# Optimization experiments

Measured on AMD Instinct MI355X. Metric: run time of the kernel, lower is better.

Reference implementation:

```python
import jax, jax.numpy as jnp
import numpy as np

N_E = 4096
E_DIM = 64
BETA = 0.25


def setup_inputs() -> dict:
    key = jax.random.key(0)
    k1, k2 = jax.random.split(key)
    z = jax.random.normal(k1, (16, E_DIM, 32, 32), dtype=jnp.float32)
    embedding = jax.random.normal(k2, (N_E, E_DIM), dtype=jnp.float32)
    return {"z": z, "embedding": embedding}


def reference(z, embedding):
    # b c h w -> b h w c
    zc = jnp.transpose(z, (0, 2, 3, 1))  # [B,H,W,C]
    B, H, W, C = zc.shape
    zf = zc.reshape(-1, C)  # [N, C]

    # Squared Euclidean distances (argmin is identical to cdist p=2 argmin)
    # d2[n,e] = |z|^2 - 2 z.e + |e|^2
    d2 = (
        jnp.sum(zf * zf, axis=1, keepdims=True)
        - 2.0 * (zf @ embedding.T)
        + jnp.sum(embedding * embedding, axis=1)[None, :]
    )  # [N, n_e]
    idx = jnp.argmin(d2, axis=1)  # [N]

    z_q = embedding[idx].reshape(B, H, W, C)

    # dist_p == 2 losses
    loss_d1 = jnp.mean((jax.lax.stop_gradient(z_q) - zc) ** 2)
    loss_d2 = jnp.mean((z_q - jax.lax.stop_gradient(zc)) ** 2)
    loss = BETA * loss_d1 + loss_d2

    # Straight-through estimator
    z_q = zc + jax.lax.stop_gradient(z_q - zc)

    indices = idx.reshape(B, H, W)
    z_q = jnp.transpose(z_q, (0, 3, 1, 2))  # b h w c -> b c h w
    return z_q, loss, indices
```

## Files before the change

### kernel.cpp

```cpp
#include <hip/hip_runtime.h>

typedef float f32x4 __attribute__((ext_vector_type(4)));
typedef float f32x16 __attribute__((ext_vector_type(16)));
typedef short bf16x8 __attribute__((ext_vector_type(8)));

#define HW_ 1024
#define NE_ 4096
#define CHW_ 65536
#define ZQ_SIZE 1048576
#define LOSS_OFF ZQ_SIZE
#define IDX_OFF (ZQ_SIZE + 1)
#define LOSS_SCALE (1.25f / 1048576.f)
#define EPS_GAP 0.1f

union FragU { unsigned u[4]; bf16x8 v; };

__device__ __forceinline__ unsigned umin_(unsigned a, unsigned b) { return a < b ? a : b; }
__device__ __forceinline__ unsigned umax_(unsigned a, unsigned b) { return a > b ? a : b; }

__device__ __forceinline__ void top2_(unsigned key, unsigned& s1, unsigned& s2) {
    unsigned t;
    asm("v_med3_u32 %0, %1, %2, %3" : "=v"(t) : "v"(key), "v"(s1), "v"(s2));
    s2 = t;
    s1 = umin_(s1, key);
}

__device__ __forceinline__ void split8(const float* v, FragU& hi, FragU& lo) {
#pragma unroll
    for (int p = 0; p < 4; p++) {
        float a = v[2 * p], b = v[2 * p + 1];
        unsigned ua = __float_as_uint(a), ub = __float_as_uint(b);
        hi.u[p] = (ua >> 16) | (ub & 0xFFFF0000u);
        float la = a - __uint_as_float(ua & 0xFFFF0000u);
        float lb = b - __uint_as_float(ub & 0xFFFF0000u);
        lo.u[p] = (__float_as_uint(la) >> 16) | (__float_as_uint(lb) & 0xFFFF0000u);
    }
}

__device__ __forceinline__ void gload_lds16(const void* g, void* l) {
    __builtin_amdgcn_global_load_lds(
        (const __attribute__((address_space(1))) unsigned*)g,
        (__attribute__((address_space(3))) unsigned*)l, 16, 0, 0);
}

__global__ __launch_bounds__(256) void vq_eprep(
        const float* __restrict__ emb, char* __restrict__ efrag,
        float* __restrict__ h_e, float* __restrict__ out) {
    const int bid = blockIdx.x, tid = threadIdx.x;
    if (bid < 128) {
        int u = bid * 256 + tid;
        int l = u & 63, ks = (u >> 6) & 3, t = u >> 8;
        int erow = t * 32 + (l & 31);
        int k0 = ks * 16 + (l >> 5) * 8;
        const float* ep = emb + (size_t)erow * 64 + k0;
        float4 ea = *(const float4*)(ep);
        float4 eb = *(const float4*)(ep + 4);
        float v[8];
        v[0] = -ea.x; v[1] = -ea.y; v[2] = -ea.z; v[3] = -ea.w;
        v[4] = -eb.x; v[5] = -eb.y; v[6] = -eb.z; v[7] = -eb.w;
        FragU hi, lo;
        split8(v, hi, lo);
        char* base = efrag + (size_t)t * 8192 + ks * 1024 + l * 16;
        *(FragU*)(base)        = hi;
        *(FragU*)(base + 4096) = lo;
    } else {
        int t = (bid - 128) * 256 + tid;
        const float4* er = (const float4*)(emb + (size_t)t * 64);
        float s = 0.f;
#pragma unroll
        for (int k = 0; k < 16; k++) {
            float4 e4 = er[k];
            s = fmaf(e4.x, e4.x, s); s = fmaf(e4.y, e4.y, s);
            s = fmaf(e4.z, e4.z, s); s = fmaf(e4.w, e4.w, s);
        }
        h_e[t] = 0.5f * s;
        if (t == 0) out[LOSS_OFF] = 0.f;
    }
}

__global__ __launch_bounds__(512) void vq_mfma(
        const float* __restrict__ z, const char* __restrict__ efrag,
        const float* __restrict__ h_e,
        unsigned* __restrict__ k1q, unsigned* __restrict__ k2q) {
    __shared__ char buf[2][32768];
    __shared__ __attribute__((aligned(16))) float sh_he[512];

    const int tid = threadIdx.x;
    const int lane = tid & 63;
    const int w = tid >> 6;
    const int col = lane & 31;
    const int kgrp = lane >> 5;
    const int es = blockIdx.x >> 5;
    const int rb = blockIdx.x & 31;
    const int e0t = es * 16;
    const int b = rb >> 1;
    const int row0 = rb * 512 + w * 64;

    sh_he[tid] = h_e[es * 512 + tid];

    {
        const char* src = efrag + (size_t)(e0t + (w >> 1)) * 8192
                          + (w & 1) * 4096 + lane * 16;
        char* dst = buf[0] + (w >> 1) * 8192 + (w & 1) * 4096;
#pragma unroll
        for (int i = 0; i < 4; i++) gload_lds16(src + i * 1024, dst + i * 1024);
    }

    bf16x8 Zh[2][4], Zl[2][4];
    float hzv[2];
#pragma unroll
    for (int zt = 0; zt < 2; zt++) {
        float ss = 0.f;
        const int hw = ((rb & 1) << 9) + w * 64 + zt * 32 + col;
        const float* zp = z + (size_t)b * CHW_ + hw;
#pragma unroll
        for (int ks = 0; ks < 4; ks++) {
            const int c0 = ks * 16 + kgrp * 8;
            float v[8];
#pragma unroll
            for (int j = 0; j < 8; j++) {
                v[j] = zp[(c0 + j) * HW_];
                ss = fmaf(v[j], v[j], ss);
            }
            FragU hi, lo;
            split8(v, hi, lo);
            Zh[zt][ks] = hi.v;
            Zl[zt][ks] = lo.v;
        }
        ss += __shfl_xor(ss, 32);
        hzv[zt] = 0.5f * ss;
    }

    unsigned s1k[2] = {~0u, ~0u};
    unsigned s2k[2] = {~0u, ~0u};

    __syncthreads();
    for (int c = 0; c < 4; c++) {
        if (c < 3) {
            const char* src = efrag + (size_t)(e0t + (c + 1) * 4 + (w >> 1)) * 8192
                              + (w & 1) * 4096 + lane * 16;
            char* dst = buf[(c + 1) & 1] + (w >> 1) * 8192 + (w & 1) * 4096;
#pragma unroll
            for (int i = 0; i < 4; i++) gload_lds16(src + i * 1024, dst + i * 1024);
        }

#pragma unroll
        for (int jt = 0; jt < 4; jt++) {
            const char* tb = buf[c & 1] + jt * 8192 + lane * 16;
            bf16x8 Ah[4], Al[4];
#pragma unroll
            for (int ks = 0; ks < 4; ks++) {
                Ah[ks] = *(const bf16x8*)(tb + ks * 1024);
                Al[ks] = *(const bf16x8*)(tb + 4096 + ks * 1024);
            }
            const int tloc = c * 4 + jt;
            f32x4 he[4];
#pragma unroll
            for (int rq = 0; rq < 4; rq++)
                he[rq] = *(const f32x4*)&sh_he[tloc * 32 + 8 * rq + 4 * kgrp];

            f32x16 c0, c1;
#pragma unroll
            for (int rq = 0; rq < 4; rq++)
#pragma unroll
                for (int rr = 0; rr < 4; rr++) {
                    c0[rq * 4 + rr] = he[rq][rr] + hzv[0];
                    c1[rq * 4 + rr] = he[rq][rr] + hzv[1];
                }

#pragma unroll
            for (int ks = 0; ks < 4; ks++) {
                c0 = __builtin_amdgcn_mfma_f32_32x32x16_bf16(Ah[ks], Zh[0][ks], c0, 0, 0, 0);
                c1 = __builtin_amdgcn_mfma_f32_32x32x16_bf16(Ah[ks], Zh[1][ks], c1, 0, 0, 0);
            }
#pragma unroll
            for (int ks = 0; ks < 4; ks++) {
                c0 = __builtin_amdgcn_mfma_f32_32x32x16_bf16(Al[ks], Zh[0][ks], c0, 0, 0, 0);
                c1 = __builtin_amdgcn_mfma_f32_32x32x16_bf16(Al[ks], Zh[1][ks], c1, 0, 0, 0);
            }
#pragma unroll
            for (int ks = 0; ks < 4; ks++) {
                c0 = __builtin_amdgcn_mfma_f32_32x32x16_bf16(Ah[ks], Zl[0][ks], c0, 0, 0, 0);
                c1 = __builtin_amdgcn_mfma_f32_32x32x16_bf16(Ah[ks], Zl[1][ks], c1, 0, 0, 0);
            }

            const unsigned eb = (unsigned)(es * 512 + tloc * 32 + 4 * kgrp);
#pragma unroll
            for (int rq = 0; rq < 4; rq++)
#pragma unroll
                for (int rr = 0; rr < 4; rr++) {
                    const unsigned eo = eb + rr + 8 * rq;
                    top2_((__float_as_uint(c0[rq * 4 + rr]) & 0xFFFFF000u) | eo, s1k[0], s2k[0]);
                    top2_((__float_as_uint(c1[rq * 4 + rr]) & 0xFFFFF000u) | eo, s1k[1], s2k[1]);
                }
        }
        __syncthreads();
    }

#pragma unroll
    for (int r = 0; r < 2; r++) {
        unsigned o1 = (unsigned)__shfl_xor((int)s1k[r], 32);
        unsigned o2 = (unsigned)__shfl_xor((int)s2k[r], 32);
        s2k[r] = umin_(umin_(s2k[r], o2), umax_(s1k[r], o1));
        s1k[r] = umin_(s1k[r], o1);
    }

    if (lane < 32) {
        const int base = es * 16384 + row0;
#pragma unroll
        for (int r = 0; r < 2; r++) {
            k1q[base + r * 32 + lane] = s1k[r];
            k2q[base + r * 32 + lane] = s2k[r];
        }
    }
}

__global__ __launch_bounds__(256) void vq_final(
        const float* __restrict__ z, const float* __restrict__ emb,
        const unsigned* __restrict__ k1q, const unsigned* __restrict__ k2q,
        float* __restrict__ out) {
    int t = blockIdx.x * 256 + threadIdx.x;
    int n = t & 16383;
    int q = t >> 14;

    unsigned m = 0xFFFFFFFFu, s = 0xFFFFFFFFu;
#pragma unroll
    for (int i = 0; i < 8; i++) {
        unsigned a = k1q[i * 16384 + n];
        unsigned b = k2q[i * 16384 + n];
        unsigned hi = umax_(m, a);
        m = umin_(m, a);
        s = umin_(umin_(s, b), hi);
    }

    int idx = (int)(m & 0xFFFu);
    float s1 = __uint_as_float(m & 0xFFFFF000u);
    float s2 = __uint_as_float(s & 0xFFFFF000u);

    int b = n >> 10, hw = n & 1023;
    const float* zp = z + (size_t)b * CHW_ + hw;
    const int cq = q * 16;

    if (s2 - s1 < EPS_GAP) {
        int i2 = (int)(s & 0xFFFu);
        const float* ea = emb + (size_t)idx * 64;
        const float* eb = emb + (size_t)i2 * 64;
        double da = 0.0, db = 0.0;
#pragma unroll 8
        for (int c = 0; c < 64; c++) {
            double zv = (double)zp[c * HW_];
            double xa = (double)ea[c] - zv;
            double xb = (double)eb[c] - zv;
            da = fma(xa, xa, da);
            db = fma(xb, xb, db);
        }
        if (db < da || (db == da && i2 < idx)) idx = i2;
    }

    const float* er = emb + (size_t)idx * 64 + cq;
    float* zq = out + (size_t)b * CHW_ + hw;
    float lsum = 0.f;
#pragma unroll
    for (int j = 0; j < 16; j++) {
        float e = er[j];
        float d = e - zp[(cq + j) * HW_];
        zq[(cq + j) * HW_] = e;
        lsum = fmaf(d, d, lsum);
    }
    if (q == 0) out[IDX_OFF + n] = (float)idx;

#pragma unroll
    for (int off = 32; off; off >>= 1) lsum += __shfl_down(lsum, off);
    if ((threadIdx.x & 63) == 0) atomicAdd(&out[LOSS_OFF], lsum * LOSS_SCALE);
}

extern "C" void kernel_launch(void* const* d_in, const int* in_sizes, int n_in,
                              void* d_out, int out_size, void* d_ws, size_t ws_size,
                              hipStream_t stream) {
    const float* z   = (const float*)d_in[0];
    const float* emb = (const float*)d_in[1];
    float* out = (float*)d_out;
    char* ws = (char*)d_ws;

    char* efrag   = ws;
    float* h_e    = (float*)(ws + 1048576);
    unsigned* k1q = (unsigned*)(ws + 1065024);
    unsigned* k2q = (unsigned*)(ws + 1589312);

    vq_eprep<<<144, 256, 0, stream>>>(emb, efrag, h_e, out);
    vq_mfma <<<256, 512, 0, stream>>>(z, efrag, h_e, k1q, k2q);
    vq_final<<<256, 256, 0, stream>>>(z, emb, k1q, k2q, out);
}
```

Before: 50.79 us.

## Fuse three VQ kernels into one cooperative kernel with grid syncs

Merges the embedding prep, MFMA distance/top-2 search, and final gather/loss kernels into a single cooperative launch separated by grid-wide barriers. This removes two kernel launch boundaries and their inter-kernel gaps. In exchange it adds grid.sync overhead, leaves only half the threads busy in the final phase, and requires all 256 blocks of 512 threads to be co-resident.

Measured after the change: 193.6 us. 3.81x slower.

```diff
diff --git a/kernel.cpp b/kernel.cpp
--- a/kernel.cpp
+++ b/kernel.cpp
@@ -1,4 +1,7 @@
 #include <hip/hip_runtime.h>
+#include <hip/hip_cooperative_groups.h>
+
+namespace cg = cooperative_groups;
 
 typedef float f32x4 __attribute__((ext_vector_type(4)));
 typedef float f32x16 __attribute__((ext_vector_type(16)));
@@ -43,51 +46,55 @@
         (__attribute__((address_space(3))) unsigned*)l, 16, 0, 0);
 }
 
-__global__ __launch_bounds__(256) void vq_eprep(
-        const float* __restrict__ emb, char* __restrict__ efrag,
-        float* __restrict__ h_e, float* __restrict__ out) {
-    const int bid = blockIdx.x, tid = threadIdx.x;
-    if (bid < 128) {
-        int u = bid * 256 + tid;
-        int l = u & 63, ks = (u >> 6) & 3, t = u >> 8;
-        int erow = t * 32 + (l & 31);
-        int k0 = ks * 16 + (l >> 5) * 8;
-        const float* ep = emb + (size_t)erow * 64 + k0;
-        float4 ea = *(const float4*)(ep);
-        float4 eb = *(const float4*)(ep + 4);
-        float v[8];
-        v[0] = -ea.x; v[1] = -ea.y; v[2] = -ea.z; v[3] = -ea.w;
-        v[4] = -eb.x; v[5] = -eb.y; v[6] = -eb.z; v[7] = -eb.w;
-        FragU hi, lo;
-        split8(v, hi, lo);
-        char* base = efrag + (size_t)t * 8192 + ks * 1024 + l * 16;
-        *(FragU*)(base)        = hi;
-        *(FragU*)(base + 4096) = lo;
-    } else {
-        int t = (bid - 128) * 256 + tid;
-        const float4* er = (const float4*)(emb + (size_t)t * 64);
-        float s = 0.f;
-#pragma unroll
-        for (int k = 0; k < 16; k++) {
-            float4 e4 = er[k];
-            s = fmaf(e4.x, e4.x, s); s = fmaf(e4.y, e4.y, s);
-            s = fmaf(e4.z, e4.z, s); s = fmaf(e4.w, e4.w, s);
-        }
-        h_e[t] = 0.5f * s;
-        if (t == 0) out[LOSS_OFF] = 0.f;
-    }
-}
-
-__global__ __launch_bounds__(512) void vq_mfma(
-        const float* __restrict__ z, const char* __restrict__ efrag,
-        const float* __restrict__ h_e,
-        unsigned* __restrict__ k1q, unsigned* __restrict__ k2q) {
+__global__ __launch_bounds__(512) void vq_all(
+        const float* __restrict__ z, const float* __restrict__ emb,
+        char* __restrict__ efrag, float* __restrict__ h_e,
+        unsigned* __restrict__ k1q, unsigned* __restrict__ k2q,
+        float* __restrict__ out) {
     __shared__ char buf[2][32768];
     __shared__ __attribute__((aligned(16))) float sh_he[512];
+
+    cg::grid_group grid = cg::this_grid();
 
     const int tid = threadIdx.x;
     const int lane = tid & 63;
     const int w = tid >> 6;
+
+    {
+        int gid = blockIdx.x * 512 + tid;
+        if (gid < 32768) {
+            int l = gid & 63, ks = (gid >> 6) & 3, t = gid >> 8;
+            int erow = t * 32 + (l & 31);
+            int k0 = ks * 16 + (l >> 5) * 8;
+            const float* ep = emb + (size_t)erow * 64 + k0;
+            float4 ea = *(const float4*)(ep);
+            float4 eb = *(const float4*)(ep + 4);
+            float v[8];
+            v[0] = -ea.x; v[1] = -ea.y; v[2] = -ea.z; v[3] = -ea.w;
+            v[4] = -eb.x; v[5] = -eb.y; v[6] = -eb.z; v[7] = -eb.w;
+            FragU hi, lo;
+            split8(v, hi, lo);
+            char* base = efrag + (size_t)t * 8192 + ks * 1024 + l * 16;
+            *(FragU*)(base)        = hi;
+            *(FragU*)(base + 4096) = lo;
+        } else if (gid < 36864) {
+            int t = gid - 32768;
+            const float4* er = (const float4*)(emb + (size_t)t * 64);
+            float s = 0.f;
+#pragma unroll
+            for (int k = 0; k < 16; k++) {
+                float4 e4 = er[k];
+                s = fmaf(e4.x, e4.x, s); s = fmaf(e4.y, e4.y, s);
+                s = fmaf(e4.z, e4.z, s); s = fmaf(e4.w, e4.w, s);
+            }
+            h_e[t] = 0.5f * s;
+        } else if (gid == 36864) {
+            out[LOSS_OFF] = 0.f;
+        }
+    }
+    __threadfence();
+    grid.sync();
+
     const int col = lane & 31;
     const int kgrp = lane >> 5;
     const int es = blockIdx.x >> 5;
@@ -213,65 +220,65 @@
             k2q[base + r * 32 + lane] = s2k[r];
         }
     }
-}
-
-__global__ __launch_bounds__(256) void vq_final(
-        const float* __restrict__ z, const float* __restrict__ emb,
-        const unsigned* __restrict__ k1q, const unsigned* __restrict__ k2q,
-        float* __restrict__ out) {
-    int t = blockIdx.x * 256 + threadIdx.x;
-    int n = t & 16383;
-    int q = t >> 14;
-
-    unsigned m = 0xFFFFFFFFu, s = 0xFFFFFFFFu;
-#pragma unroll
-    for (int i = 0; i < 8; i++) {
-        unsigned a = k1q[i * 16384 + n];
-        unsigned b = k2q[i * 16384 + n];
-        unsigned hi = umax_(m, a);
-        m = umin_(m, a);
-        s = umin_(umin_(s, b), hi);
-    }
-
-    int idx = (int)(m & 0xFFFu);
-    float s1 = __uint_as_float(m & 0xFFFFF000u);
-    float s2 = __uint_as_float(s & 0xFFFFF000u);
-
-    int b = n >> 10, hw = n & 1023;
-    const float* zp = z + (size_t)b * CHW_ + hw;
-    const int cq = q * 16;
-
-    if (s2 - s1 < EPS_GAP) {
-        int i2 = (int)(s & 0xFFFu);
-        const float* ea = emb + (size_t)idx * 64;
-        const float* eb = emb + (size_t)i2 * 64;
-        double da = 0.0, db = 0.0;
+
+    __threadfence();
+    grid.sync();
+
+    if (tid < 256) {
+        int t = blockIdx.x * 256 + tid;
+        int n = t & 16383;
+        int q = t >> 14;
+
+        unsigned m = 0xFFFFFFFFu, s = 0xFFFFFFFFu;
+#pragma unroll
+        for (int i = 0; i < 8; i++) {
+            unsigned a = k1q[i * 16384 + n];
+            unsigned bb = k2q[i * 16384 + n];
+            unsigned hi = umax_(m, a);
+            m = umin_(m, a);
+            s = umin_(umin_(s, bb), hi);
+        }
+
+        int idx = (int)(m & 0xFFFu);
+        float sc1 = __uint_as_float(m & 0xFFFFF000u);
+        float sc2 = __uint_as_float(s & 0xFFFFF000u);
+
+        int bb2 = n >> 10, hw = n & 1023;
+        const float* zp = z + (size_t)bb2 * CHW_ + hw;
+        const int cq = q * 16;
+
+        if (sc2 - sc1 < EPS_GAP) {
+            int i2 = (int)(s & 0xFFFu);
+            const float* ea = emb + (size_t)idx * 64;
+            const float* eb2 = emb + (size_t)i2 * 64;
+            double da = 0.0, db = 0.0;
 #pragma unroll 8
-        for (int c = 0; c < 64; c++) {
-            double zv = (double)zp[c * HW_];
-            double xa = (double)ea[c] - zv;
-            double xb = (double)eb[c] - zv;
-            da = fma(xa, xa, da);
-            db = fma(xb, xb, db);
-        }
-        if (db < da || (db == da && i2 < idx)) idx = i2;
-    }
-
-    const float* er = emb + (size_t)idx * 64 + cq;
-    float* zq = out + (size_t)b * CHW_ + hw;
-    float lsum = 0.f;
-#pragma unroll
-    for (int j = 0; j < 16; j++) {
-        float e = er[j];
-        float d = e - zp[(cq + j) * HW_];
-        zq[(cq + j) * HW_] = e;
-        lsum = fmaf(d, d, lsum);
-    }
-    if (q == 0) out[IDX_OFF + n] = (float)idx;
-
-#pragma unroll
-    for (int off = 32; off; off >>= 1) lsum += __shfl_down(lsum, off);
-    if ((threadIdx.x & 63) == 0) atomicAdd(&out[LOSS_OFF], lsum * LOSS_SCALE);
+            for (int c = 0; c < 64; c++) {
+                double zv = (double)zp[c * HW_];
+                double xa = (double)ea[c] - zv;
+                double xb = (double)eb2[c] - zv;
+                da = fma(xa, xa, da);
+                db = fma(xb, xb, db);
+            }
+            if (db < da || (db == da && i2 < idx)) idx = i2;
+        }
+
+        const float* er = emb + (size_t)idx * 64 + cq;
+        float* zq = out + (size_t)bb2 * CHW_ + hw;
+        float lsum = 0.f;
+#pragma unroll
+        for (int j = 0; j < 16; j++) {
+            float e = er[j];
+            float d = e - zp[(cq + j) * HW_];
+            zq[(cq + j) * HW_] = e;
+            lsum = fmaf(d, d, lsum);
+        }
+        if (q == 0) out[IDX_OFF + n] = (float)idx;
+
+#pragma unroll
+        for (int off = 32; off; off >>= 1) lsum += __shfl_down(lsum, off);
+        if ((tid & 63) == 0) atomicAdd(&out[LOSS_OFF], lsum * LOSS_SCALE);
+    }
 }
 
 extern "C" void kernel_launch(void* const* d_in, const int* in_sizes, int n_in,
@@ -287,7 +294,8 @@
     unsigned* k1q = (unsigned*)(ws + 1065024);
     unsigned* k2q = (unsigned*)(ws + 1589312);
 
-    vq_eprep<<<144, 256, 0, stream>>>(emb, efrag, h_e, out);
-    vq_mfma <<<256, 512, 0, stream>>>(z, efrag, h_e, k1q, k2q);
-    vq_final<<<256, 256, 0, stream>>>(z, emb, k1q, k2q, out);
-}
+    void* args[] = {(void*)&z, (void*)&emb, (void*)&efrag, (void*)&h_e,
+                    (void*)&k1q, (void*)&k2q, (void*)&out};
+    hipLaunchCooperativeKernel((const void*)vq_all, dim3(256), dim3(512),
+                               args, 0, stream);
+}
```
